# Kernel tuning notes

Hardware: AMD Instinct MI355X
Metric: run time of the kernel (lower is better)

Reference implementation:

```python
import jax, jax.numpy as jnp
import numpy as np

TOP_P = 0.95        # sample() default topp
TEMPERATURE = 0.8   # token_temperature
NEG_INF = float('-inf')


def setup_inputs() -> dict:
    key = jax.random.key(0)
    k1, k2 = jax.random.split(key)
    B, V = 8192, 2048  # batch rows x speech-unit vocab
    logits = jax.random.normal(k1, (B, V), dtype=jnp.float32) * 4.0
    # uniform noise for Gumbel-max multinomial sampling (open interval)
    u = jax.random.uniform(k2, (B, V), dtype=jnp.float32, minval=1e-6, maxval=1.0 - 1e-6)
    return {"logits": logits, "u": u}


def _top_p_filter(logits, p):
    # descending sort (matches torch.sort(descending=True))
    order = jnp.argsort(-logits, axis=-1)                      # [B, V]
    sorted_logits = jnp.take_along_axis(logits, order, axis=-1)
    cum = jnp.cumsum(jax.nn.softmax(sorted_logits, axis=-1), axis=-1)
    remove = cum > p
    # shift right by one so the first token above the threshold is kept
    remove = jnp.concatenate(
        [jnp.zeros_like(remove[..., :1]), remove[..., :-1]], axis=-1)
    # scatter mask back to unsorted order via inverse permutation
    inv = jnp.argsort(order, axis=-1)
    remove_unsorted = jnp.take_along_axis(remove, inv, axis=-1)
    return jnp.where(remove_unsorted, NEG_INF, logits)


def reference(logits, u):
    scaled = logits / TEMPERATURE
    filtered = _top_p_filter(scaled, TOP_P)                    # [B, V]
    probs = jax.nn.softmax(filtered, axis=-1)                  # [B, V]
    # multinomial(probs, 1) == Gumbel-max over filtered logits
    gumbel = -jnp.log(-jnp.log(u))
    sampled = jnp.argmax(filtered + gumbel, axis=-1, keepdims=True)  # [B, 1]
    return sampled, probs
```

## Files before the change

kernel.cpp:

```cpp
#include <hip/hip_runtime.h>
#include <math.h>

#define VOCAB 2048
#define TPB   256
#define NBINS 64
#define BIN_SCALE 6.0f

__global__ __launch_bounds__(TPB) void sampler_kernel(
    const float* __restrict__ logits,
    const float* __restrict__ uni,
    float* __restrict__ out_idx,
    float* __restrict__ out_probs)
{
    const int row  = blockIdx.x;
    const int t    = threadIdx.x;
    const int lane = t & 63;
    const int wid  = t >> 6;

    __shared__ float  s_bins[NBINS];
    __shared__ float  s_wf[4];
    __shared__ double s_wd[4];
    __shared__ float  s_m;
    __shared__ double s_S;
    __shared__ double s_SK;
    __shared__ double s_cumBefore;
    __shared__ int    s_bstar;
    __shared__ int    s_cnt;
    __shared__ float  s_cv[VOCAB];
    __shared__ float  s_ce[VOCAB];
    __shared__ float  s_rz[4];
    __shared__ int    s_ri[4];

    const float* lrow = logits   + (size_t)row * VOCAB;
    const float* urow = uni      + (size_t)row * VOCAB;
    float*       prow = out_probs + (size_t)row * VOCAB;

    if (t < NBINS) s_bins[t] = 0.0f;
    if (t == 0)    s_cnt = 0;

    float4 a0 = *(const float4*)(lrow + 4 * t);
    float4 a1 = *(const float4*)(lrow + VOCAB / 2 + 4 * t);
    float s[8];
    s[0] = a0.x / 0.8f; s[1] = a0.y / 0.8f; s[2] = a0.z / 0.8f; s[3] = a0.w / 0.8f;
    s[4] = a1.x / 0.8f; s[5] = a1.y / 0.8f; s[6] = a1.z / 0.8f; s[7] = a1.w / 0.8f;

    float lm = s[0];
    #pragma unroll
    for (int j = 1; j < 8; j++) lm = fmaxf(lm, s[j]);
    #pragma unroll
    for (int off = 32; off; off >>= 1) lm = fmaxf(lm, __shfl_down(lm, off));
    if (lane == 0) s_wf[wid] = lm;
    __syncthreads();
    if (t == 0) s_m = fmaxf(fmaxf(s_wf[0], s_wf[1]), fmaxf(s_wf[2], s_wf[3]));
    __syncthreads();
    const float m = s_m;

    float e[8];
    int   bin[8];
    float psum = 0.0f;
    #pragma unroll
    for (int j = 0; j < 8; j++) {
        e[j] = expf(s[j] - m);
        psum += e[j];
        bin[j] = (int)((m - s[j]) * BIN_SCALE);
        if (bin[j] < NBINS) atomicAdd(&s_bins[bin[j]], e[j]);
    }
    double dp = (double)psum;
    #pragma unroll
    for (int off = 32; off; off >>= 1) dp += __shfl_down(dp, off);
    if (lane == 0) s_wd[wid] = dp;
    __syncthreads();
    if (t == 0) {
        double S  = s_wd[0] + s_wd[1] + s_wd[2] + s_wd[3];
        double pS = 0.95 * S;
        double cum = 0.0, cb = 0.0;
        int bstar = -1;
        for (int b = 0; b < NBINS; b++) {
            double nc = cum + (double)s_bins[b];
            if (bstar < 0 && nc > pS) { bstar = b; cb = cum; }
            cum = nc;
        }
        if (bstar < 0) { bstar = NBINS - 1; cb = cum - (double)s_bins[NBINS - 1]; }
        s_S = S; s_bstar = bstar; s_cumBefore = cb;
    }
    __syncthreads();
    const double S         = s_S;
    const double pS        = 0.95 * S;
    const int    bstar     = s_bstar;
    const double cumBefore = s_cumBefore;

    #pragma unroll
    for (int j = 0; j < 8; j++) {
        if (bin[j] == bstar) {
            int pos = atomicAdd(&s_cnt, 1);
            s_cv[pos] = s[j];
            s_ce[pos] = e[j];
        }
    }
    __syncthreads();
    const int cnt = s_cnt;

    unsigned keptMask = 0;
    float    kpsum    = 0.0f;
    #pragma unroll
    for (int j = 0; j < 8; j++) {
        bool kept;
        if (bin[j] < bstar)      kept = true;
        else if (bin[j] > bstar) kept = false;
        else {
            float part = 0.0f;
            for (int i = 0; i < cnt; i++)
                if (s_cv[i] > s[j]) part += s_ce[i];
            kept = (cumBefore + (double)part) <= pS;
        }
        if (kept) { keptMask |= (1u << j); kpsum += e[j]; }
    }

    double dk = (double)kpsum;
    #pragma unroll
    for (int off = 32; off; off >>= 1) dk += __shfl_down(dk, off);
    if (lane == 0) s_wd[wid] = dk;
    __syncthreads();
    if (t == 0) s_SK = s_wd[0] + s_wd[1] + s_wd[2] + s_wd[3];
    __syncthreads();
    const float SK = (float)s_SK;

    float4 p0, p1;
    p0.x = (keptMask & 0x01) ? e[0] / SK : 0.0f;
    p0.y = (keptMask & 0x02) ? e[1] / SK : 0.0f;
    p0.z = (keptMask & 0x04) ? e[2] / SK : 0.0f;
    p0.w = (keptMask & 0x08) ? e[3] / SK : 0.0f;
    p1.x = (keptMask & 0x10) ? e[4] / SK : 0.0f;
    p1.y = (keptMask & 0x20) ? e[5] / SK : 0.0f;
    p1.z = (keptMask & 0x40) ? e[6] / SK : 0.0f;
    p1.w = (keptMask & 0x80) ? e[7] / SK : 0.0f;
    *(float4*)(prow + 4 * t)             = p0;
    *(float4*)(prow + VOCAB / 2 + 4 * t) = p1;

    float4 u0 = *(const float4*)(urow + 4 * t);
    float4 u1 = *(const float4*)(urow + VOCAB / 2 + 4 * t);
    float uu[8] = {u0.x, u0.y, u0.z, u0.w, u1.x, u1.y, u1.z, u1.w};
    float bz = -INFINITY;
    int   bi = 0x7fffffff;
    #pragma unroll
    for (int j = 0; j < 8; j++) {
        if ((keptMask >> j) & 1u) {
            float g   = -logf(-logf(uu[j]));
            float z   = s[j] + g;
            int   idx = (j < 4) ? (4 * t + j) : (VOCAB / 2 + 4 * t + (j - 4));
            if (z > bz || (z == bz && idx < bi)) { bz = z; bi = idx; }
        }
    }
    #pragma unroll
    for (int off = 32; off; off >>= 1) {
        float oz = __shfl_down(bz, off);
        int   oi = __shfl_down(bi, off);
        if (oz > bz || (oz == bz && oi < bi)) { bz = oz; bi = oi; }
    }
    if (lane == 0) { s_rz[wid] = bz; s_ri[wid] = bi; }
    __syncthreads();
    if (t == 0) {
        float z0 = s_rz[0]; int i0 = s_ri[0];
        for (int w = 1; w < 4; w++) {
            if (s_rz[w] > z0 || (s_rz[w] == z0 && s_ri[w] < i0)) { z0 = s_rz[w]; i0 = s_ri[w]; }
        }
        out_idx[row] = (float)i0;
    }
}

extern "C" void kernel_launch(void* const* d_in, const int* in_sizes, int n_in,
                              void* d_out, int out_size, void* d_ws, size_t ws_size,
                              hipStream_t stream) {
    const float* logits = (const float*)d_in[0];
    const float* u      = (const float*)d_in[1];
    const int B = in_sizes[0] / VOCAB;
    float* out_idx   = (float*)d_out;
    float* out_probs = (float*)d_out + B;
    sampler_kernel<<<B, TPB, 0, stream>>>(logits, u, out_idx, out_probs);
}
```

Measured before the change: 172.5 us.

## Compact kept tokens before Gumbel sampling and gather only their noise values

Kept tokens (set by top-p) are compacted into shared memory, and the uniform noise is gathered only for those indices. This skips the full-row read of u and the log work on discarded tokens. The change also replaces the serial single-thread bin scan with a wave-wide shuffle prefix scan plus ballot, drops several barriers, and uses a float reduction for the kept sum. It also uses fast exp, multiplies by a reciprocal, adds nontemporal stores, and packs (value, index) into a 64-bit key for the argmax reduction. The cost is scattered 4-byte gathers from u and an extra barrier and atomic pass.

```diff
diff --git a/kernel.cpp b/kernel.cpp
--- a/kernel.cpp
+++ b/kernel.cpp
@@ -6,7 +6,9 @@
 #define NBINS 64
 #define BIN_SCALE 6.0f
 
-__global__ __launch_bounds__(TPB) void sampler_kernel(
+typedef float vf4 __attribute__((ext_vector_type(4)));
+
+__global__ __launch_bounds__(TPB, 8) void sampler_kernel(
     const float* __restrict__ logits,
     const float* __restrict__ uni,
     float* __restrict__ out_idx,
@@ -20,29 +22,24 @@
     __shared__ float  s_bins[NBINS];
     __shared__ float  s_wf[4];
     __shared__ double s_wd[4];
-    __shared__ float  s_m;
-    __shared__ double s_S;
-    __shared__ double s_SK;
-    __shared__ double s_cumBefore;
-    __shared__ int    s_bstar;
-    __shared__ int    s_cnt;
+    __shared__ float  s_wk[4];
+    __shared__ unsigned long long s_key[4];
+    __shared__ double s_S, s_cumBefore;
+    __shared__ int    s_bstar, s_cnt, s_cnt2;
     __shared__ float  s_cv[VOCAB];
     __shared__ float  s_ce[VOCAB];
-    __shared__ float  s_rz[4];
-    __shared__ int    s_ri[4];
 
-    const float* lrow = logits   + (size_t)row * VOCAB;
-    const float* urow = uni      + (size_t)row * VOCAB;
+    const float* lrow = logits    + (size_t)row * VOCAB;
+    const float* urow = uni       + (size_t)row * VOCAB;
     float*       prow = out_probs + (size_t)row * VOCAB;
 
     if (t < NBINS) s_bins[t] = 0.0f;
-    if (t == 0)    s_cnt = 0;
+    if (t == 0)    { s_cnt = 0; s_cnt2 = 0; }
 
-    float4 a0 = *(const float4*)(lrow + 4 * t);
-    float4 a1 = *(const float4*)(lrow + VOCAB / 2 + 4 * t);
-    float s[8];
-    s[0] = a0.x / 0.8f; s[1] = a0.y / 0.8f; s[2] = a0.z / 0.8f; s[3] = a0.w / 0.8f;
-    s[4] = a1.x / 0.8f; s[5] = a1.y / 0.8f; s[6] = a1.z / 0.8f; s[7] = a1.w / 0.8f;
+    const vf4 a0 = *(const vf4*)(lrow + 4 * t);
+    const vf4 a1 = *(const vf4*)(lrow + VOCAB / 2 + 4 * t);
+    float s[8] = {a0.x * 1.25f, a0.y * 1.25f, a0.z * 1.25f, a0.w * 1.25f,
+                  a1.x * 1.25f, a1.y * 1.25f, a1.z * 1.25f, a1.w * 1.25f};
 
     float lm = s[0];
     #pragma unroll
@@ -51,16 +48,14 @@
     for (int off = 32; off; off >>= 1) lm = fmaxf(lm, __shfl_down(lm, off));
     if (lane == 0) s_wf[wid] = lm;
     __syncthreads();
-    if (t == 0) s_m = fmaxf(fmaxf(s_wf[0], s_wf[1]), fmaxf(s_wf[2], s_wf[3]));
-    __syncthreads();
-    const float m = s_m;
+    const float m = fmaxf(fmaxf(s_wf[0], s_wf[1]), fmaxf(s_wf[2], s_wf[3]));
 
     float e[8];
     int   bin[8];
     float psum = 0.0f;
     #pragma unroll
     for (int j = 0; j < 8; j++) {
-        e[j] = expf(s[j] - m);
+        e[j] = __expf(s[j] - m);
         psum += e[j];
         bin[j] = (int)((m - s[j]) * BIN_SCALE);
         if (bin[j] < NBINS) atomicAdd(&s_bins[bin[j]], e[j]);
@@ -70,22 +65,25 @@
     for (int off = 32; off; off >>= 1) dp += __shfl_down(dp, off);
     if (lane == 0) s_wd[wid] = dp;
     __syncthreads();
-    if (t == 0) {
+
+    if (wid == 0) {
         double S  = s_wd[0] + s_wd[1] + s_wd[2] + s_wd[3];
+        float  bf = s_bins[lane];
+        double c  = (double)bf;
+        #pragma unroll
+        for (int d = 1; d < 64; d <<= 1) {
+            double o = __shfl_up(c, d);
+            if (lane >= d) c += o;
+        }
         double pS = 0.95 * S;
-        double cum = 0.0, cb = 0.0;
-        int bstar = -1;
-        for (int b = 0; b < NBINS; b++) {
-            double nc = cum + (double)s_bins[b];
-            if (bstar < 0 && nc > pS) { bstar = b; cb = cum; }
-            cum = nc;
-        }
-        if (bstar < 0) { bstar = NBINS - 1; cb = cum - (double)s_bins[NBINS - 1]; }
-        s_S = S; s_bstar = bstar; s_cumBefore = cb;
+        unsigned long long ball = __ballot(c > pS);
+        int bstar = ball ? (__ffsll(ball) - 1) : (NBINS - 1);
+        double excl = c - (double)bf;
+        double cumB = __shfl(excl, bstar);
+        if (lane == 0) { s_S = S; s_bstar = bstar; s_cumBefore = cumB; }
     }
     __syncthreads();
-    const double S         = s_S;
-    const double pS        = 0.95 * S;
+    const double pS        = 0.95 * s_S;
     const int    bstar     = s_bstar;
     const double cumBefore = s_cumBefore;
 
@@ -115,56 +113,62 @@
         }
         if (kept) { keptMask |= (1u << j); kpsum += e[j]; }
     }
+    #pragma unroll
+    for (int off = 32; off; off >>= 1) kpsum += __shfl_down(kpsum, off);
+    if (lane == 0) s_wk[wid] = kpsum;
+    __syncthreads();
+    const float SK    = s_wk[0] + s_wk[1] + s_wk[2] + s_wk[3];
+    const float invSK = 1.0f / SK;
 
-    double dk = (double)kpsum;
-    #pragma unroll
-    for (int off = 32; off; off >>= 1) dk += __shfl_down(dk, off);
-    if (lane == 0) s_wd[wid] = dk;
-    __syncthreads();
-    if (t == 0) s_SK = s_wd[0] + s_wd[1] + s_wd[2] + s_wd[3];
-    __syncthreads();
-    const float SK = (float)s_SK;
+    vf4 p0, p1;
+    p0.x = (keptMask & 0x01) ? e[0] * invSK : 0.0f;
+    p0.y = (keptMask & 0x02) ? e[1] * invSK : 0.0f;
+    p0.z = (keptMask & 0x04) ? e[2] * invSK : 0.0f;
+    p0.w = (keptMask & 0x08) ? e[3] * invSK : 0.0f;
+    p1.x = (keptMask & 0x10) ? e[4] * invSK : 0.0f;
+    p1.y = (keptMask & 0x20) ? e[5] * invSK : 0.0f;
+    p1.z = (keptMask & 0x40) ? e[6] * invSK : 0.0f;
+    p1.w = (keptMask & 0x80) ? e[7] * invSK : 0.0f;
+    __builtin_nontemporal_store(p0, (vf4*)(prow + 4 * t));
+    __builtin_nontemporal_store(p1, (vf4*)(prow + VOCAB / 2 + 4 * t));
 
-    float4 p0, p1;
-    p0.x = (keptMask & 0x01) ? e[0] / SK : 0.0f;
-    p0.y = (keptMask & 0x02) ? e[1] / SK : 0.0f;
-    p0.z = (keptMask & 0x04) ? e[2] / SK : 0.0f;
-    p0.w = (keptMask & 0x08) ? e[3] / SK : 0.0f;
-    p1.x = (keptMask & 0x10) ? e[4] / SK : 0.0f;
-    p1.y = (keptMask & 0x20) ? e[5] / SK : 0.0f;
-    p1.z = (keptMask & 0x40) ? e[6] / SK : 0.0f;
-    p1.w = (keptMask & 0x80) ? e[7] / SK : 0.0f;
-    *(float4*)(prow + 4 * t)             = p0;
-    *(float4*)(prow + VOCAB / 2 + 4 * t) = p1;
-
-    float4 u0 = *(const float4*)(urow + 4 * t);
-    float4 u1 = *(const float4*)(urow + VOCAB / 2 + 4 * t);
-    float uu[8] = {u0.x, u0.y, u0.z, u0.w, u1.x, u1.y, u1.z, u1.w};
-    float bz = -INFINITY;
-    int   bi = 0x7fffffff;
     #pragma unroll
     for (int j = 0; j < 8; j++) {
         if ((keptMask >> j) & 1u) {
-            float g   = -logf(-logf(uu[j]));
-            float z   = s[j] + g;
-            int   idx = (j < 4) ? (4 * t + j) : (VOCAB / 2 + 4 * t + (j - 4));
-            if (z > bz || (z == bz && idx < bi)) { bz = z; bi = idx; }
+            int idx = (j < 4) ? (4 * t + j) : (VOCAB / 2 + 4 * t + (j - 4));
+            int pos = atomicAdd(&s_cnt2, 1);
+            s_cv[pos] = s[j];
+            s_ce[pos] = __int_as_float(idx);
         }
+    }
+    __syncthreads();
+    const int k = s_cnt2;
+
+    unsigned long long key = 0ull;
+    for (int i = t; i < k; i += TPB) {
+        float sv  = s_cv[i];
+        int   idx = __float_as_int(s_ce[i]);
+        float uv  = urow[idx];
+        float g   = -logf(-logf(uv));
+        float z   = sv + g;
+        unsigned zb = __float_as_uint(z);
+        zb = (zb & 0x80000000u) ? ~zb : (zb | 0x80000000u);
+        unsigned long long kk =
+            ((unsigned long long)zb << 32) | (unsigned)(VOCAB - 1 - idx);
+        key = (kk > key) ? kk : key;
     }
     #pragma unroll
     for (int off = 32; off; off >>= 1) {
-        float oz = __shfl_down(bz, off);
-        int   oi = __shfl_down(bi, off);
-        if (oz > bz || (oz == bz && oi < bi)) { bz = oz; bi = oi; }
+        unsigned long long ok = __shfl_down(key, off);
+        key = (ok > key) ? ok : key;
     }
-    if (lane == 0) { s_rz[wid] = bz; s_ri[wid] = bi; }
+    if (lane == 0) s_key[wid] = key;
     __syncthreads();
     if (t == 0) {
-        float z0 = s_rz[0]; int i0 = s_ri[0];
-        for (int w = 1; w < 4; w++) {
-            if (s_rz[w] > z0 || (s_rz[w] == z0 && s_ri[w] < i0)) { z0 = s_rz[w]; i0 = s_ri[w]; }
-        }
-        out_idx[row] = (float)i0;
+        unsigned long long k0 = s_key[0];
+        #pragma unroll
+        for (int w = 1; w < 4; w++) k0 = (s_key[w] > k0) ? s_key[w] : k0;
+        out_idx[row] = (float)(VOCAB - 1 - (int)(k0 & 0xFFFFFFFFu));
     }
 }
 
```

Result: faster. 164.5 us (-4.7%).
